# Kernel optimization log

Hardware: AMD Instinct MI355X
Metric: run time of the kernel (lower is better)

## Reference

```python
import jax, jax.numpy as jnp
import numpy as np

NUM_EXPERTS = 8


def setup_inputs() -> dict:
    key = jax.random.key(0)
    k1, k2, k3, k4 = jax.random.split(key, 4)
    d_model, d_ff, E = 768, 3072, NUM_EXPERTS
    B, S = 4, 1024
    scale_in = 1.0 / np.sqrt(d_model)
    scale_ff = 1.0 / np.sqrt(d_ff)
    return {
        "hidden_states": jax.random.normal(k1, (B, S, d_model), dtype=jnp.float32),
        "router_weight": jax.random.normal(k2, (d_model, E), dtype=jnp.float32) * scale_in,
        "wi": jax.random.normal(k3, (E, d_model, d_ff), dtype=jnp.float32) * scale_in,
        "wo": jax.random.normal(k4, (E, d_ff, d_model), dtype=jnp.float32) * scale_ff,
    }


def reference(hidden_states, router_weight, wi, wo):
    # --- Top-1 router (HF computes softmax in fp32) ---
    router_logits = jnp.einsum("bsd,de->bse", hidden_states.astype(jnp.float32), router_weight.astype(jnp.float32))  # [B,S,E]
    probs = jax.nn.softmax(router_logits, axis=-1)
    expert_index = jnp.argmax(probs, axis=-1)                      # [B,S] int
    router_mask = jax.nn.one_hot(expert_index, NUM_EXPERTS, dtype=probs.dtype)  # [B,S,E]
    router_probs = jnp.max(probs, axis=-1, keepdims=True).astype(hidden_states.dtype)  # [B,S,1]

    # --- Experts: dense per-expert MLP, combined by the one-hot top-1 mask.
    # Every token is routed to exactly one expert, so masked-sum == dispatch/combine.
    h = jax.nn.relu(jnp.einsum("bsd,edf->bsef", hidden_states, wi))  # [B,S,E,d_ff]
    y = jnp.einsum("bsef,efd->bsed", h, wo)                           # [B,S,E,d_model]
    next_states = jnp.einsum("bse,bsed->bsd", router_mask.astype(hidden_states.dtype), y)

    out = router_probs * next_states
    return out, router_logits, expert_index
```

## Files before the change

### kernel.cpp

```cpp
#include <hip/hip_runtime.h>


typedef __attribute__((ext_vector_type(4))) float f32x4;
typedef __attribute__((ext_vector_type(8))) short short8;
typedef unsigned short ushort_t;
typedef unsigned int uint32;

#define DEVFN static __device__ __forceinline__
#define MFMA __builtin_amdgcn_mfma_f32_16x16x32_bf16

constexpr int NTOK = 4096;
constexpr int DM   = 768;
constexpr int DF   = 3072;
constexpr int NE   = 8;
constexpr int TM   = 128;
constexpr int MAXTILES = NTOK / TM + NE;
constexpr int MAXR  = MAXTILES * TM;
constexpr int BK    = 32;
constexpr int KS2   = 2;

DEVFN ushort_t f2bf(float f) {
  uint32 u = __float_as_uint(f);
  u += 0x7fffu + ((u >> 16) & 1u);
  return (ushort_t)(u >> 16);
}
DEVFN float bf2f(ushort_t u) { return __uint_as_float((uint32)u << 16); }
DEVFN uint32 pkbf(float a, float b) {
  return (__float_as_uint(b) & 0xffff0000u) | (__float_as_uint(a) >> 16);
}

DEVFN void gl16(const void* g, void* l) {
  __builtin_amdgcn_global_load_lds(
      (const __attribute__((address_space(1))) void*)g,
      (__attribute__((address_space(3))) void*)l, 16, 0, 0);
}

__global__ __launch_bounds__(256) void k_router(
    const float* __restrict__ X, const float* __restrict__ Wr,
    float* __restrict__ out_logits, float* __restrict__ out_idx,
    int* __restrict__ expert_of, float* __restrict__ prob) {
  int wid = threadIdx.x >> 6, lane = threadIdx.x & 63;
  int t = blockIdx.x * 4 + wid;
  const float* xrow = X + (size_t)t * DM;
  double acc[NE];
#pragma unroll
  for (int e = 0; e < NE; e++) acc[e] = 0.0;
  for (int d0 = 0; d0 < DM; d0 += 64) {
    int d = d0 + lane;
    float x = xrow[d];
    const float4* w4 = (const float4*)(Wr + (size_t)d * NE);
    float4 wa = w4[0], wb = w4[1];
    acc[0] += (double)x * wa.x; acc[1] += (double)x * wa.y;
    acc[2] += (double)x * wa.z; acc[3] += (double)x * wa.w;
    acc[4] += (double)x * wb.x; acc[5] += (double)x * wb.y;
    acc[6] += (double)x * wb.z; acc[7] += (double)x * wb.w;
  }
#pragma unroll
  for (int e = 0; e < NE; e++) {
#pragma unroll
    for (int s = 32; s > 0; s >>= 1) acc[e] += __shfl_xor(acc[e], s);
  }
#pragma unroll
  for (int e = 0; e < NE; e++)
    if (lane == e) out_logits[(size_t)t * NE + e] = (float)acc[e];
  double m = acc[0]; int idx = 0;
#pragma unroll
  for (int e = 1; e < NE; e++) if (acc[e] > m) { m = acc[e]; idx = e; }
  float s = 0.f;
#pragma unroll
  for (int e = 0; e < NE; e++) s += expf((float)(acc[e] - m));
  if (lane == 0) {
    out_idx[t] = (float)idx;
    expert_of[t] = idx;
    prob[t] = 1.f / s;
  }
}

__global__ __launch_bounds__(64) void k_scan(
    const int* __restrict__ expert_of, const float* __restrict__ prob,
    int* __restrict__ meta, int* __restrict__ perm,
    float* __restrict__ prob_g) {
  __shared__ int exl[NTOK];
  int lane = threadIdx.x;
  const int4* src = (const int4*)expert_of;
  int4* dst = (int4*)exl;
#pragma unroll
  for (int j = 0; j < NTOK / 4 / 64; j++) dst[j * 64 + lane] = src[j * 64 + lane];
  __syncthreads();
  int cnt[NE];
#pragma unroll
  for (int e = 0; e < NE; e++) cnt[e] = 0;
  for (int j = 0; j < 64; j++) {
    int ex = exl[lane * 64 + j];
#pragma unroll
    for (int e = 0; e < NE; e++) cnt[e] += (ex == e);
  }
  int base[NE], tot[NE];
#pragma unroll
  for (int e = 0; e < NE; e++) {
    int inc = cnt[e];
#pragma unroll
    for (int s = 1; s < 64; s <<= 1) {
      int o = __shfl_up(inc, s);
      if (lane >= s) inc += o;
    }
    base[e] = inc - cnt[e];
    tot[e] = __shfl(inc, 63);
  }
  int segStart[NE];
  int pos = 0, nt = 0;
#pragma unroll
  for (int e = 0; e < NE; e++) {
    segStart[e] = pos;
    int tiles = (tot[e] + TM - 1) / TM;
    if (lane == 0) {
      meta[8 + e] = pos;
      meta[16 + e] = pos + tot[e];
      for (int i = 0; i < tiles; i++) {
        meta[64 + nt + i] = e;
        meta[128 + nt + i] = pos + i * TM;
      }
    }
    nt += tiles;
    pos += tiles * TM;
  }
  if (lane == 0) meta[24] = nt;
  int cum[NE];
#pragma unroll
  for (int e = 0; e < NE; e++) cum[e] = segStart[e] + base[e];
  for (int j = 0; j < 64; j++) {
    int t = lane * 64 + j;
    int ex = exl[lane * 64 + j];
    int p = 0;
#pragma unroll
    for (int e = 0; e < NE; e++) p += (ex == e) ? cum[e] : 0;
#pragma unroll
    for (int e = 0; e < NE; e++) cum[e] += (ex == e);
    perm[p] = t;
    prob_g[p] = prob[t];
  }
}

__global__ __launch_bounds__(256) void k_copy(
    const float* __restrict__ X, const int* __restrict__ meta,
    const int* __restrict__ perm, ushort_t* __restrict__ Xg) {
  int bt = blockIdx.y;
  if (bt >= meta[24]) return;
  int e = meta[64 + bt], row0 = meta[128 + bt], segEnd = meta[16 + e];
  int wid = threadIdx.x >> 6, lane = threadIdx.x & 63;
  int r = row0 + blockIdx.x * 4 + wid;
  if (r >= segEnd) return;
  int tok = perm[r];
  const float2* s2 = (const float2*)(X + (size_t)tok * DM);
  uint32* d2 = (uint32*)(Xg + (size_t)r * DM);
#pragma unroll
  for (int i = 0; i < DM / 128; i++) {
    float2 v = s2[i * 64 + lane];
    d2[i * 64 + lane] = (uint32)f2bf(v.x) | ((uint32)f2bf(v.y) << 16);
  }
}

template <int KTOT, int NB, int KSPLIT, bool FIRST>
__global__ __launch_bounds__(256, 3) void k_gemm8(
    const ushort_t* __restrict__ A, const float* __restrict__ Bw,
    const int* __restrict__ meta, ushort_t* __restrict__ Obf) {
  constexpr int NKTT = KTOT / KSPLIT / BK;
  __shared__ short A_lds[2][128 * BK];
  __shared__ short B_lds[2][128 * BK];

  int bt = blockIdx.y;
  if (bt >= meta[24]) return;
  int e    = meta[64 + bt];
  int row0 = meta[128 + bt];
  int n0, koff, z;
  if constexpr (FIRST) {
    n0 = blockIdx.x * 128; koff = 0; z = 0;
  } else {
    n0 = (blockIdx.x / KSPLIT) * 128; z = blockIdx.x % KSPLIT;
    koff = z * (KTOT / KSPLIT);
  }

  int tid = threadIdx.x, lane = tid & 63, w = tid >> 6;
  int wr = w >> 1, wc = w & 1;

  int srcSlot = (lane & 3) ^ ((lane >> 3) & 3);
  const ushort_t* aS = A + (size_t)(row0 + (tid >> 2)) * KTOT + koff + srcSlot * 8;
  int dstOff = w * 512;

#define STAGE_A(buf, kt)                                                      \
  do {                                                                        \
    gl16(aS + (size_t)(kt) * BK, &A_lds[buf][dstOff]);                        \
    gl16(aS + (size_t)(kt) * BK + (size_t)64 * KTOT,                          \
         &A_lds[buf][dstOff + 2048]);                                         \
  } while (0)

  int kq = tid >> 5, nc = tid & 31;
  const float* bS = Bw + (size_t)e * KTOT * NB + ((size_t)koff + kq * 4) * NB
                    + n0 + nc;
  float bv[4][4];

#define LOAD_B(kt)                                                            \
  do {                                                                        \
    const float* b0 = bS + (size_t)(kt) * BK * NB;                            \
    _Pragma("unroll") for (int kk = 0; kk < 4; kk++)                          \
      _Pragma("unroll") for (int nn = 0; nn < 4; nn++)                        \
        bv[kk][nn] = b0[(size_t)kk * NB + nn * 32];                           \
  } while (0)

#define WRITE_B(buf)                                                          \
  do {                                                                        \
    _Pragma("unroll") for (int nn = 0; nn < 4; nn++) {                        \
      int c = nc + 32 * nn;                                                   \
      int sg = (c ^ (c >> 2)) & 3;                                            \
      int ad = c * BK + (((kq >> 1) ^ sg) << 3) + ((kq & 1) << 2);            \
      uint32 w0 = pkbf(bv[0][nn], bv[1][nn]);                                 \
      uint32 w1 = pkbf(bv[2][nn], bv[3][nn]);                                 \
      *(uint2*)&B_lds[buf][ad] = (uint2){w0, w1};                             \
    }                                                                         \
  } while (0)

  int g = lane >> 4;
  int kslotRd = (g ^ ((lane >> 1) & 3)) * 8;
  int aOff[4], bOff[4];
#pragma unroll
  for (int m = 0; m < 4; m++)
    aOff[m] = (wr * 64 + m * 16 + (lane & 15)) * BK + kslotRd;
#pragma unroll
  for (int n = 0; n < 4; n++) {
    int col = wc * 64 + n * 16 + (lane & 15);
    int sg = (col ^ (col >> 2)) & 3;
    bOff[n] = col * BK + ((g ^ sg) << 3);
  }

  f32x4 acc[4][4];
#pragma unroll
  for (int m = 0; m < 4; m++)
#pragma unroll
    for (int n = 0; n < 4; n++) acc[m][n] = (f32x4){0.f, 0.f, 0.f, 0.f};

  LOAD_B(0);
  STAGE_A(0, 0);
  WRITE_B(0);
  __syncthreads();

#pragma unroll 2
  for (int t = 0; t < NKTT; ++t) {
    int cur = t & 1;
    if (t + 1 < NKTT) {
      LOAD_B(t + 1);
      STAGE_A(cur ^ 1, t + 1);
    }
    const short* aB = A_lds[cur];
    const short* bB = B_lds[cur];
    short8 af[4], bf[4];
#pragma unroll
    for (int m = 0; m < 4; m++) af[m] = *(const short8*)&aB[aOff[m]];
#pragma unroll
    for (int n = 0; n < 4; n++) bf[n] = *(const short8*)&bB[bOff[n]];
    __builtin_amdgcn_s_setprio(1);
#pragma unroll
    for (int m = 0; m < 4; m++)
#pragma unroll
      for (int n = 0; n < 4; n++)
        acc[m][n] = MFMA(af[m], bf[n], acc[m][n], 0, 0, 0);
    __builtin_amdgcn_s_setprio(0);
    if (t + 1 < NKTT) WRITE_B(cur ^ 1);
    __syncthreads();
  }
#undef STAGE_A
#undef LOAD_B
#undef WRITE_B

  ushort_t* dst = FIRST ? Obf : Obf + (size_t)z * MAXR * NB;
#pragma unroll
  for (int m = 0; m < 4; m++) {
    int rowb = row0 + wr * 64 + m * 16 + (lane >> 4) * 4;
#pragma unroll
    for (int n = 0; n < 4; n++) {
      int col = n0 + wc * 64 + n * 16 + (lane & 15);
#pragma unroll
      for (int r = 0; r < 4; r++) {
        float v = acc[m][n][r];
        if (FIRST) v = v > 0.f ? v : 0.f;
        dst[(size_t)(rowb + r) * NB + col] = f2bf(v);
      }
    }
  }
}

__global__ __launch_bounds__(256) void k_reduce(
    const ushort_t* __restrict__ P, const int* __restrict__ meta,
    const int* __restrict__ perm, const float* __restrict__ prob_g,
    float* __restrict__ out) {
  int bt = blockIdx.y;
  if (bt >= meta[24]) return;
  int e = meta[64 + bt], row0 = meta[128 + bt], segEnd = meta[16 + e];
  int c0 = blockIdx.x * 64;
  int t = threadIdx.x;
  int col = c0 + (t & 7) * 8;
#pragma unroll
  for (int i = 0; i < 4; i++) {
    int r = row0 + (t >> 3) + i * 32;
    if (r >= segEnd) continue;
    int tok = perm[r];
    float p = prob_g[r];
    float s[8];
#pragma unroll
    for (int j = 0; j < 8; j++) s[j] = 0.f;
#pragma unroll
    for (int z = 0; z < KS2; z++) {
      short8 v = *(const short8*)&P[((size_t)z * MAXR + r) * DM + col];
#pragma unroll
      for (int j = 0; j < 8; j++) s[j] += bf2f((ushort_t)v[j]);
    }
    float4 o0 = {p * s[0], p * s[1], p * s[2], p * s[3]};
    float4 o1 = {p * s[4], p * s[5], p * s[6], p * s[7]};
    *(float4*)&out[(size_t)tok * DM + col] = o0;
    *(float4*)&out[(size_t)tok * DM + col + 4] = o1;
  }
}

extern "C" void kernel_launch(void* const* d_in, const int* in_sizes, int n_in,
                              void* d_out, int out_size, void* d_ws, size_t ws_size,
                              hipStream_t stream) {
  const float* X  = (const float*)d_in[0];
  const float* Wr = (const float*)d_in[1];
  const float* wi = (const float*)d_in[2];
  const float* wo = (const float*)d_in[3];

  float* out        = (float*)d_out;
  float* out_logits = out + (size_t)NTOK * DM;
  float* out_idx    = out_logits + (size_t)NTOK * NE;

  char* w = (char*)d_ws;
  int*      meta      = (int*)w;
  int*      expert_of = (int*)(w + 4096);
  float*    prob      = (float*)(w + 20480);
  int*      perm      = (int*)(w + 36864);
  float*    prob_g    = (float*)(w + 61440);
  ushort_t* Xg        = (ushort_t*)(w + 131072);
  ushort_t* H         = Xg + (size_t)MAXR * DM;
  ushort_t* P         = H + (size_t)MAXR * DF;

  k_router<<<NTOK / 4, 256, 0, stream>>>(X, Wr, out_logits, out_idx,
                                         expert_of, prob);
  k_scan<<<1, 64, 0, stream>>>(expert_of, prob, meta, perm, prob_g);
  k_copy<<<dim3(TM / 4, MAXTILES), 256, 0, stream>>>(X, meta, perm, Xg);
  k_gemm8<DM, DF, 1, true><<<dim3(DF / 128, MAXTILES), 256, 0, stream>>>(
      Xg, wi, meta, H);
  k_gemm8<DF, DM, KS2, false><<<dim3((DM / 128) * KS2, MAXTILES), 256, 0, stream>>>(
      H, wo, meta, P);
  k_reduce<<<dim3(DM / 64, MAXTILES), 256, 0, stream>>>(P, meta, perm, prob_g, out);
}
```

Measured before the change: 139.1 us.

## Deepen B prefetch pipeline, flatten grouped GEMM grid, raise second GEMM K-split to 4

The GEMM main loop is fully unrolled over 24 K-steps with two register banks for B, so B global loads run two steps ahead. Explicit vmcnt waits plus raw s_barrier replace __syncthreads. The grid is flattened to 1D with tile index as the fast dimension, so blocks that share weights (same expert and column) run close together and the inactive tail blocks exit as one contiguous range. The second GEMM's K split goes from 2 to 4 to give more parallelism, at the cost of more partial-sum traffic in the reduce kernel. The hand-tuned vmcnt counts depend on the compiler emitting loads in a specific order, and the static_assert fixes NKT at 24.

Result: slower. 177.2 us (+27.4%).

```diff
diff --git a/kernel.cpp b/kernel.cpp
--- a/kernel.cpp
+++ b/kernel.cpp
@@ -17,7 +17,7 @@
 constexpr int MAXTILES = NTOK / TM + NE;
 constexpr int MAXR  = MAXTILES * TM;
 constexpr int BK    = 32;
-constexpr int KS2   = 2;
+constexpr int KS    = 4;
 
 DEVFN ushort_t f2bf(float f) {
   uint32 u = __float_as_uint(f);
@@ -164,20 +164,23 @@
 __global__ __launch_bounds__(256, 3) void k_gemm8(
     const ushort_t* __restrict__ A, const float* __restrict__ Bw,
     const int* __restrict__ meta, ushort_t* __restrict__ Obf) {
-  constexpr int NKTT = KTOT / KSPLIT / BK;
+  static_assert(KTOT / KSPLIT / BK == 24, "NKT must be 24");
+  constexpr int NPZ = (NB / 128) * KSPLIT;
   __shared__ short A_lds[2][128 * BK];
   __shared__ short B_lds[2][128 * BK];
 
-  int bt = blockIdx.y;
-  if (bt >= meta[24]) return;
-  int e    = meta[64 + bt];
-  int row0 = meta[128 + bt];
+  int nt = meta[24];
+  unsigned lin = blockIdx.x;
+  if (lin >= (unsigned)(nt * NPZ)) return;
+  int tile = lin % (unsigned)nt;
+  int pz   = lin / (unsigned)nt;
+  int e    = meta[64 + tile];
+  int row0 = meta[128 + tile];
   int n0, koff, z;
   if constexpr (FIRST) {
-    n0 = blockIdx.x * 128; koff = 0; z = 0;
+    n0 = pz * 128; koff = 0; z = 0;
   } else {
-    n0 = (blockIdx.x / KSPLIT) * 128; z = blockIdx.x % KSPLIT;
-    koff = z * (KTOT / KSPLIT);
+    n0 = (pz >> 2) * 128; z = pz & 3; koff = z * (KTOT / KSPLIT);
   }
 
   int tid = threadIdx.x, lane = tid & 63, w = tid >> 6;
@@ -197,24 +200,24 @@
   int kq = tid >> 5, nc = tid & 31;
   const float* bS = Bw + (size_t)e * KTOT * NB + ((size_t)koff + kq * 4) * NB
                     + n0 + nc;
-  float bv[4][4];
-
-#define LOAD_B(kt)                                                            \
+  float bvA[4][4], bvB[4][4];
+
+#define LOAD_B(dst, kt)                                                       \
   do {                                                                        \
     const float* b0 = bS + (size_t)(kt) * BK * NB;                            \
     _Pragma("unroll") for (int kk = 0; kk < 4; kk++)                          \
       _Pragma("unroll") for (int nn = 0; nn < 4; nn++)                        \
-        bv[kk][nn] = b0[(size_t)kk * NB + nn * 32];                           \
-  } while (0)
-
-#define WRITE_B(buf)                                                          \
+        dst[kk][nn] = b0[(size_t)kk * NB + nn * 32];                          \
+  } while (0)
+
+#define WRITE_B(buf, src)                                                     \
   do {                                                                        \
     _Pragma("unroll") for (int nn = 0; nn < 4; nn++) {                        \
       int c = nc + 32 * nn;                                                   \
       int sg = (c ^ (c >> 2)) & 3;                                            \
       int ad = c * BK + (((kq >> 1) ^ sg) << 3) + ((kq & 1) << 2);            \
-      uint32 w0 = pkbf(bv[0][nn], bv[1][nn]);                                 \
-      uint32 w1 = pkbf(bv[2][nn], bv[3][nn]);                                 \
+      uint32 w0 = pkbf(src[0][nn], src[1][nn]);                               \
+      uint32 w1 = pkbf(src[2][nn], src[3][nn]);                               \
       *(uint2*)&B_lds[buf][ad] = (uint2){w0, w1};                             \
     }                                                                         \
   } while (0)
@@ -238,35 +241,53 @@
 #pragma unroll
     for (int n = 0; n < 4; n++) acc[m][n] = (f32x4){0.f, 0.f, 0.f, 0.f};
 
-  LOAD_B(0);
+#define FRAGS_MFMA(ab, bb)                                                    \
+  do {                                                                        \
+    short8 af[4], bf[4];                                                      \
+    _Pragma("unroll") for (int m = 0; m < 4; m++)                             \
+      af[m] = *(const short8*)&(ab)[aOff[m]];                                 \
+    _Pragma("unroll") for (int n = 0; n < 4; n++)                             \
+      bf[n] = *(const short8*)&(bb)[bOff[n]];                                 \
+    __builtin_amdgcn_s_setprio(1);                                            \
+    _Pragma("unroll") for (int m = 0; m < 4; m++)                             \
+      _Pragma("unroll") for (int n = 0; n < 4; n++)                           \
+        acc[m][n] = MFMA(af[m], bf[n], acc[m][n], 0, 0, 0);                   \
+    __builtin_amdgcn_s_setprio(0);                                            \
+  } while (0)
+
+#define KSTEP(T, CUR, NXT)                                                    \
+  do {                                                                        \
+    STAGE_A(((T) + 1) & 1, (T) + 1);                           \
+    LOAD_B(NXT, (T) + 2);                                      \
+    FRAGS_MFMA(A_lds[(T) & 1], B_lds[(T) & 1]);                               \
+    asm volatile("s_waitcnt vmcnt(18)" ::: "memory");        \
+    WRITE_B(((T) + 1) & 1, CUR);                                              \
+    asm volatile("s_waitcnt vmcnt(16) lgkmcnt(0)" ::: "memory");  \
+    __builtin_amdgcn_s_barrier();                        \
+  } while (0)
+
+  LOAD_B(bvA, 0);
   STAGE_A(0, 0);
-  WRITE_B(0);
-  __syncthreads();
-
-#pragma unroll 2
-  for (int t = 0; t < NKTT; ++t) {
-    int cur = t & 1;
-    if (t + 1 < NKTT) {
-      LOAD_B(t + 1);
-      STAGE_A(cur ^ 1, t + 1);
-    }
-    const short* aB = A_lds[cur];
-    const short* bB = B_lds[cur];
-    short8 af[4], bf[4];
-#pragma unroll
-    for (int m = 0; m < 4; m++) af[m] = *(const short8*)&aB[aOff[m]];
-#pragma unroll
-    for (int n = 0; n < 4; n++) bf[n] = *(const short8*)&bB[bOff[n]];
-    __builtin_amdgcn_s_setprio(1);
-#pragma unroll
-    for (int m = 0; m < 4; m++)
-#pragma unroll
-      for (int n = 0; n < 4; n++)
-        acc[m][n] = MFMA(af[m], bf[n], acc[m][n], 0, 0, 0);
-    __builtin_amdgcn_s_setprio(0);
-    if (t + 1 < NKTT) WRITE_B(cur ^ 1);
-    __syncthreads();
-  }
+  asm volatile("s_waitcnt vmcnt(2)" ::: "memory");
+  WRITE_B(0, bvA);
+  LOAD_B(bvB, 1);
+  asm volatile("s_waitcnt vmcnt(16) lgkmcnt(0)" ::: "memory");
+  __builtin_amdgcn_s_barrier();
+
+#pragma unroll
+  for (int t2 = 0; t2 < 22; t2 += 2) {
+    KSTEP(t2,     bvB, bvA);
+    KSTEP(t2 + 1, bvA, bvB);
+  }
+  STAGE_A(1, 23);
+  FRAGS_MFMA(A_lds[0], B_lds[0]);
+  asm volatile("s_waitcnt vmcnt(2)" ::: "memory");
+  WRITE_B(1, bvB);
+  asm volatile("s_waitcnt vmcnt(0) lgkmcnt(0)" ::: "memory");
+  __builtin_amdgcn_s_barrier();
+  FRAGS_MFMA(A_lds[1], B_lds[1]);
+#undef KSTEP
+#undef FRAGS_MFMA
 #undef STAGE_A
 #undef LOAD_B
 #undef WRITE_B
@@ -308,7 +329,7 @@
 #pragma unroll
     for (int j = 0; j < 8; j++) s[j] = 0.f;
 #pragma unroll
-    for (int z = 0; z < KS2; z++) {
+    for (int z = 0; z < KS; z++) {
       short8 v = *(const short8*)&P[((size_t)z * MAXR + r) * DM + col];
 #pragma unroll
       for (int j = 0; j < 8; j++) s[j] += bf2f((ushort_t)v[j]);
@@ -346,9 +367,9 @@
                                          expert_of, prob);
   k_scan<<<1, 64, 0, stream>>>(expert_of, prob, meta, perm, prob_g);
   k_copy<<<dim3(TM / 4, MAXTILES), 256, 0, stream>>>(X, meta, perm, Xg);
-  k_gemm8<DM, DF, 1, true><<<dim3(DF / 128, MAXTILES), 256, 0, stream>>>(
+  k_gemm8<DM, DF, 1, true><<<MAXTILES * 24, 256, 0, stream>>>(
       Xg, wi, meta, H);
-  k_gemm8<DF, DM, KS2, false><<<dim3((DM / 128) * KS2, MAXTILES), 256, 0, stream>>>(
+  k_gemm8<DF, DM, KS, false><<<MAXTILES * 24, 256, 0, stream>>>(
       H, wo, meta, P);
   k_reduce<<<dim3(DM / 64, MAXTILES), 256, 0, stream>>>(P, meta, perm, prob_g, out);
 }
```
